# Kernel tuning notes

Hardware: AMD Instinct MI355X
Metric: run time of the kernel (lower is better)

Reference implementation:

```python
import jax, jax.numpy as jnp
import numpy as np

WS = (8, 8)          # window size
NUM_HEADS = 16
C = 512
B_ = 2048            # batch * num_windows
NW = 256             # num_windows per image (mask dim)
N = WS[0] * WS[1]    # tokens per window = 64


def _relative_position_index():
    coords = np.stack(np.meshgrid(np.arange(WS[0]), np.arange(WS[1]), indexing='ij'))  # [2,Wh,Ww]
    flat = coords.reshape(2, -1)                         # [2,N]
    rel = flat[:, :, None] - flat[:, None, :]            # [2,N,N]
    rel = rel.transpose(1, 2, 0).astype(np.int32)        # [N,N,2]
    rel[..., 0] += WS[0] - 1
    rel[..., 1] += WS[1] - 1
    rel[..., 0] *= 2 * WS[1] - 1
    return jnp.asarray(rel.sum(-1))                      # [N,N] in [0, 225)


def setup_inputs() -> dict:
    key = jax.random.key(0)
    ks = jax.random.split(key, 8)
    return {
        'x': jax.random.normal(ks[0], (B_, N, C), jnp.float32),
        'mask': jax.random.normal(ks[1], (NW, N, N), jnp.float32),
        'qkv_w': jax.random.normal(ks[2], (3 * C, C), jnp.float32) * 0.02,
        'q_bias': jax.random.normal(ks[3], (C,), jnp.float32) * 0.02,
        'v_bias': jax.random.normal(ks[4], (C,), jnp.float32) * 0.02,
        'rpb_table': jax.random.normal(ks[5], ((2 * WS[0] - 1) * (2 * WS[1] - 1), NUM_HEADS), jnp.float32) * 0.02,
        'proj_w': jax.random.normal(ks[6], (C, C), jnp.float32) * 0.02,
        'proj_b': jax.random.normal(ks[7], (C,), jnp.float32) * 0.02,
        'rel_index': _relative_position_index(),
    }


def reference(x, mask, qkv_w, q_bias, v_bias, rpb_table, proj_w, proj_b, rel_index):
    Bw, n, c = x.shape
    h = NUM_HEADS
    d = c // h
    # qkv with bias = [q_bias, 0, v_bias]
    qkv_b = jnp.concatenate([q_bias, jnp.zeros_like(v_bias), v_bias])
    qkv = x @ qkv_w.T + qkv_b                               # [B_,N,3C]
    qkv = qkv.reshape(Bw, n, 3, h, d).transpose(2, 0, 3, 1, 4)
    q, k, v = qkv[0], qkv[1], qkv[2]                        # each [B_,h,N,d]
    scale = d ** -0.5
    attn = jnp.einsum('bhnd,bhmd->bhnm', q * scale, k)      # [B_,h,N,N]
    # gathered relative position bias
    rpb = rpb_table[rel_index.reshape(-1)].reshape(n, n, h).transpose(2, 0, 1)  # [h,N,N]
    attn = attn + rpb[None]
    nW = mask.shape[0]
    attn = attn.reshape(Bw // nW, nW, h, n, n) + mask[None, :, None]
    attn = jax.nn.softmax(attn.reshape(Bw, h, n, n), axis=-1)
    out = jnp.einsum('bhnm,bhmd->bhnd', attn, v)            # [B_,h,N,d]
    out = out.transpose(0, 2, 1, 3).reshape(Bw, n, c)
    return out @ proj_w.T + proj_b
```

## Files before the change

### kernel.cpp

```cpp
#include <hip/hip_runtime.h>

typedef short s16x8 __attribute__((ext_vector_type(8)));
typedef float f32x4 __attribute__((ext_vector_type(4)));

__device__ __forceinline__ unsigned short f2bf(float f) {
    unsigned int u = __builtin_bit_cast(unsigned int, f);
    u += 0x7fffu + ((u >> 16) & 1u);
    return (unsigned short)(u >> 16);
}

__device__ __forceinline__ void gload16(const void* g, void* l) {
    __builtin_amdgcn_global_load_lds(
        (const __attribute__((address_space(1))) unsigned int*)g,
        (__attribute__((address_space(3))) unsigned int*)l,
        16, 0, 0);
}

__global__ void cast_bf16_kernel(const float* __restrict__ src,
                                 unsigned short* __restrict__ dst, int n4) {
    int i = blockIdx.x * 256 + threadIdx.x;
    if (i >= n4) return;
    float4 v = ((const float4*)src)[i];
    ushort4 o;
    o.x = f2bf(v.x); o.y = f2bf(v.y); o.z = f2bf(v.z); o.w = f2bf(v.w);
    ((ushort4*)dst)[i] = o;
}

__global__ void rpb_kernel(const float* __restrict__ table,
                           const int* __restrict__ rel,
                           float* __restrict__ rpb) {
    int t = blockIdx.x * 64 + threadIdx.x;
    int idx = rel[t];
#pragma unroll
    for (int h = 0; h < 16; ++h)
        rpb[h * 4096 + t] = table[idx * 16 + h];
}

__device__ __forceinline__ void stage_step(const unsigned short* __restrict__ Ab,
                                           const unsigned short* __restrict__ Bb,
                                           unsigned short* base, int wave,
                                           size_t gA0, size_t gA1, int k0) {
    gload16(Ab + gA0 + k0, &base[wave * 512]);
    gload16(Ab + gA1 + k0, &base[2048 + wave * 512]);
    gload16(Bb + gA0 + k0, &base[4096 + wave * 512]);
    gload16(Bb + gA1 + k0, &base[6144 + wave * 512]);
}

template <bool SW>
__device__ __forceinline__ void mfma_step(const unsigned short* base, int ln, int hk,
                                          int wr, int wc, f32x4 (&acc)[4][4]) {
    const unsigned short* Al = base;
    const unsigned short* Bl = base + 4096;
    const int sl = hk ^ ((ln >> 1) & 3);
    s16x8 af[4], bf[4];
#pragma unroll
    for (int i = 0; i < 4; ++i)
        af[i] = *(const s16x8*)&Al[(wr + i * 16 + ln) * 32 + sl * 8];
#pragma unroll
    for (int j = 0; j < 4; ++j)
        bf[j] = *(const s16x8*)&Bl[(wc + j * 16 + ln) * 32 + sl * 8];
#pragma unroll
    for (int i = 0; i < 4; ++i)
#pragma unroll
        for (int j = 0; j < 4; ++j) {
            if constexpr (SW)
                acc[j][i] = __builtin_amdgcn_mfma_f32_16x16x32_bf16(bf[j], af[i], acc[j][i], 0, 0, 0);
            else
                acc[i][j] = __builtin_amdgcn_mfma_f32_16x16x32_bf16(af[i], bf[j], acc[i][j], 0, 0, 0);
        }
}

template <bool SW>
__device__ __forceinline__ void kloop128(const unsigned short* __restrict__ Ab,
                                         const unsigned short* __restrict__ Bb,
                                         unsigned short* smem,
                                         int t, int wave, int ln, int hk,
                                         int wr, int wc, f32x4 (&acc)[4][4]) {
    const int row = t >> 2, cg = t & 3;
    const int cgs = cg ^ ((t >> 3) & 3);
    const size_t gA0 = (size_t)row * 512 + cgs * 8;
    const size_t gA1 = (size_t)(row + 64) * 512 + cgs * 8;
    unsigned short* b0 = smem;
    unsigned short* b1 = smem + 8192;

    stage_step(Ab, Bb, b0, wave, gA0, gA1, 0);
    __syncthreads();
    for (int k0 = 0; k0 < 512; k0 += 64) {
        stage_step(Ab, Bb, b1, wave, gA0, gA1, k0 + 32);
        mfma_step<SW>(b0, ln, hk, wr, wc, acc);
        __syncthreads();
        if (k0 + 64 < 512)
            stage_step(Ab, Bb, b0, wave, gA0, gA1, k0 + 64);
        mfma_step<SW>(b1, ln, hk, wr, wc, acc);
        __syncthreads();
    }
}

template <int MODE, int NCOLS>
__global__ __launch_bounds__(256) void gemm_bt(
    const unsigned short* __restrict__ A, const unsigned short* __restrict__ B,
    const float* __restrict__ bq, const float* __restrict__ bv,
    unsigned short* __restrict__ qb, unsigned short* __restrict__ kb,
    unsigned short* __restrict__ vtb,
    const float* __restrict__ pb, float* __restrict__ out) {
    __shared__ __align__(16) unsigned short smem[16384];

    constexpr int NBN = NCOLS / 128;
    const unsigned int cpx = gridDim.x >> 3;
    const unsigned int wg = (blockIdx.x & 7u) * cpx + (blockIdx.x >> 3);
    const int bm = wg / NBN;
    const int bn = wg % NBN;
    const int t = threadIdx.x;
    const int wave = t >> 6, lane = t & 63;
    const int ln = lane & 15, hk = lane >> 4;
    const int wr = (wave >> 1) * 64, wc = (wave & 1) * 64;

    const f32x4 zero = {0.f, 0.f, 0.f, 0.f};
    f32x4 acc[4][4];
#pragma unroll
    for (int i = 0; i < 4; ++i)
#pragma unroll
        for (int j = 0; j < 4; ++j) acc[i][j] = zero;

    const unsigned short* Ab = A + (size_t)bm * 128 * 512;
    const unsigned short* Bb = B + (size_t)bn * 128 * 512;

    if constexpr (MODE == 1) {
        kloop128<true>(Ab, Bb, smem, t, wave, ln, hk, wr, wc, acc);
        float* epf = (float*)smem + wave * 1280;
#pragma unroll
        for (int j = 0; j < 4; ++j) {
            const int nn0 = bn * 128 + wc + j * 16 + hk * 4;
            const float4 b4 = *(const float4*)&pb[nn0];
#pragma unroll
            for (int i = 0; i < 4; ++i) {
                const int tk = i * 16 + ln;
                float4 o4;
                o4.x = acc[j][i][0] + b4.x;
                o4.y = acc[j][i][1] + b4.y;
                o4.z = acc[j][i][2] + b4.z;
                o4.w = acc[j][i][3] + b4.w;
                *(float4*)&epf[tk * 20 + hk * 4] = o4;
            }
            const int nnb = bn * 128 + wc + j * 16;
#pragma unroll
            for (int rr = 0; rr < 4; ++rr) {
                const int li = rr * 64 + lane;
                const int tk = li >> 2, c4 = (li & 3) * 4;
                float4 v4 = *(const float4*)&epf[tk * 20 + c4];
                *(float4*)(out + (size_t)(bm * 128 + wr + tk) * NCOLS + nnb + c4) = v4;
            }
        }
    } else {
        const int which = bn >> 2;
        const int bb = bm * 2;
        const size_t winbase = (size_t)((bb + (wr >> 6)) * 16);
        unsigned short* ep = smem + wave * 2560;
        if (which < 2) {
            kloop128<true>(Ab, Bb, smem, t, wave, ln, hk, wr, wc, acc);
            unsigned short* dst0 = (which == 0) ? qb : kb;
#pragma unroll
            for (int H = 0; H < 2; ++H) {
#pragma unroll
                for (int j2 = 0; j2 < 2; ++j2) {
                    const int j = H * 2 + j2;
                    const int rem0 = (bn * 128 + wc + j * 16 + hk * 4) & 511;
                    float4 b4 = {0.f, 0.f, 0.f, 0.f};
                    if (which == 0) b4 = *(const float4*)&bq[rem0];
                    const int ch0 = j2 * 16 + hk * 4;
#pragma unroll
                    for (int i = 0; i < 4; ++i) {
                        const int tk = i * 16 + ln;
                        ushort4 pk;
                        pk.x = f2bf(acc[j][i][0] + b4.x);
                        pk.y = f2bf(acc[j][i][1] + b4.y);
                        pk.z = f2bf(acc[j][i][2] + b4.z);
                        pk.w = f2bf(acc[j][i][3] + b4.w);
                        *(ushort4*)&ep[tk * 40 + ch0] = pk;
                    }
                }
                const int remH = (bn * 128 + wc + H * 32) & 511;
                const size_t Dq = (winbase + (remH >> 5)) * 2048;
#pragma unroll
                for (int rr = 0; rr < 4; ++rr) {
                    const int li = rr * 64 + lane;
                    const int tk = li >> 2, c8 = (li & 3) * 8;
                    s16x8 val = *(const s16x8*)&ep[tk * 40 + c8];
                    *(s16x8*)(dst0 + Dq + tk * 32 + c8) = val;
                }
            }
        } else {
            kloop128<false>(Ab, Bb, smem, t, wave, ln, hk, wr, wc, acc);
#pragma unroll
            for (int H = 0; H < 2; ++H) {
#pragma unroll
                for (int j2 = 0; j2 < 2; ++j2) {
                    const int j = H * 2 + j2;
                    const int rem = (bn * 128 + wc + j * 16 + ln) & 511;
                    const float bias = bv[rem];
                    const int ch = j2 * 16 + ln;
#pragma unroll
                    for (int i = 0; i < 4; ++i) {
                        const int tk = i * 16 + hk * 4;
                        ushort4 pk;
                        pk.x = f2bf(acc[i][j][0] + bias);
                        pk.y = f2bf(acc[i][j][1] + bias);
                        pk.z = f2bf(acc[i][j][2] + bias);
                        pk.w = f2bf(acc[i][j][3] + bias);
                        *(ushort4*)&ep[ch * 72 + tk] = pk;
                    }
                }
                const int remH = (bn * 128 + wc + H * 32) & 511;
                const size_t Dv = (winbase + (remH >> 5)) * 2048;
#pragma unroll
                for (int rr = 0; rr < 4; ++rr) {
                    const int li = rr * 64 + lane;
                    const int dd = li >> 3, t8 = (li & 7) * 8;
                    s16x8 val = *(const s16x8*)&ep[dd * 72 + t8];
                    *(s16x8*)(vtb + Dv + dd * 64 + t8) = val;
                }
            }
        }
    }
}

__global__ __launch_bounds__(256) void attn_kernel(
    const unsigned short* __restrict__ qbuf, const unsigned short* __restrict__ kbuf,
    const unsigned short* __restrict__ vtbuf, const float* __restrict__ rpb,
    const float* __restrict__ mask, unsigned short* __restrict__ aout) {
    __shared__ __align__(16) unsigned short ql[64 * 32];
    __shared__ __align__(16) unsigned short kl[64 * 32];
    __shared__ __align__(16) unsigned short vl[32 * 64];
    __shared__ __align__(16) unsigned short plds[64 * 72];

    const int bh = blockIdx.x;
    const int b = bh >> 4, head = bh & 15;
    const int wmask = b & 255;
    const int t = threadIdx.x, wave = t >> 6, lane = t & 63;
    const int ln = lane & 15, hk = lane >> 4;

    const size_t base = (size_t)bh * 2048;
    {
        const int r4 = t >> 2, c4 = t & 3;
        const int qs = c4 ^ ((t >> 3) & 3);
        gload16(qbuf + base + r4 * 32 + qs * 8, &ql[wave * 512]);
        gload16(kbuf + base + r4 * 32 + qs * 8, &kl[wave * 512]);
        const int r8 = t >> 3, c8v = t & 7;
        const int vs = c8v ^ (r8 & 7);
        gload16(vtbuf + base + r8 * 64 + vs * 8, &vl[wave * 512]);
    }
    __syncthreads();

    const f32x4 zero = {0.f, 0.f, 0.f, 0.f};
    const int slq = hk ^ ((ln >> 1) & 3);
    s16x8 aq = *(const s16x8*)&ql[(wave * 16 + ln) * 32 + slq * 8];
    f32x4 sc[4];
#pragma unroll
    for (int j = 0; j < 4; ++j) {
        s16x8 bk = *(const s16x8*)&kl[(j * 16 + ln) * 32 + slq * 8];
        sc[j] = __builtin_amdgcn_mfma_f32_16x16x32_bf16(aq, bk, zero, 0, 0, 0);
    }

    const float scale = 0.17677669529663687f;
    const float* rpb_h = rpb + head * 4096;
    const float* msk = mask + wmask * 4096;

    float p[4][4];
#pragma unroll
    for (int r = 0; r < 4; ++r) {
        const int i = wave * 16 + hk * 4 + r;
        float v[4], m = -1e30f;
#pragma unroll
        for (int j = 0; j < 4; ++j) {
            const int c = j * 16 + ln;
            v[j] = sc[j][r] * scale + rpb_h[i * 64 + c] + msk[i * 64 + c];
            m = fmaxf(m, v[j]);
        }
        for (int off = 1; off < 16; off <<= 1) m = fmaxf(m, __shfl_xor(m, off));
        float s = 0.f;
#pragma unroll
        for (int j = 0; j < 4; ++j) { v[j] = __expf(v[j] - m); s += v[j]; }
        for (int off = 1; off < 16; off <<= 1) s += __shfl_xor(s, off);
        const float inv = 1.f / s;
#pragma unroll
        for (int j = 0; j < 4; ++j) p[r][j] = v[j] * inv;
    }
#pragma unroll
    for (int r = 0; r < 4; ++r)
#pragma unroll
        for (int j = 0; j < 4; ++j)
            plds[(wave * 16 + hk * 4 + r) * 72 + j * 16 + ln] = f2bf(p[r][j]);

    f32x4 o2[2] = {zero, zero};
#pragma unroll
    for (int kt = 0; kt < 2; ++kt) {
        s16x8 ap = *(const s16x8*)&plds[(wave * 16 + ln) * 72 + kt * 32 + hk * 8];
#pragma unroll
        for (int nt = 0; nt < 2; ++nt) {
            const int vsl = (kt * 4 + hk) ^ (ln & 7);
            s16x8 bvf = *(const s16x8*)&vl[(nt * 16 + ln) * 64 + vsl * 8];
            o2[nt] = __builtin_amdgcn_mfma_f32_16x16x32_bf16(bvf, ap, o2[nt], 0, 0, 0);
        }
    }
    unsigned short* ep = plds + wave * 1152;
#pragma unroll
    for (int nt = 0; nt < 2; ++nt) {
        ushort4 pk;
        pk.x = f2bf(o2[nt][0]); pk.y = f2bf(o2[nt][1]);
        pk.z = f2bf(o2[nt][2]); pk.w = f2bf(o2[nt][3]);
        *(ushort4*)&ep[ln * 40 + nt * 16 + hk * 4] = pk;
    }
    const int tk = lane >> 2, c8 = (lane & 3) * 8;
    s16x8 val = *(const s16x8*)&ep[tk * 40 + c8];
    *(s16x8*)(aout + ((size_t)(b * 64 + wave * 16 + tk)) * 512 + head * 32 + c8) = val;
}

extern "C" void kernel_launch(void* const* d_in, const int* in_sizes, int n_in,
                              void* d_out, int out_size, void* d_ws, size_t ws_size,
                              hipStream_t stream) {
    const float* x      = (const float*)d_in[0];
    const float* mask   = (const float*)d_in[1];
    const float* qkv_w  = (const float*)d_in[2];
    const float* q_bias = (const float*)d_in[3];
    const float* v_bias = (const float*)d_in[4];
    const float* rpb_t  = (const float*)d_in[5];
    const float* proj_w = (const float*)d_in[6];
    const float* proj_b = (const float*)d_in[7];
    const int*   rel    = (const int*)d_in[8];
    float* out = (float*)d_out;

    char* ws = (char*)d_ws;
    unsigned short* xbf   = (unsigned short*)ws;
    unsigned short* qbuf  = (unsigned short*)(ws + 0x08000000);
    unsigned short* kbuf  = (unsigned short*)(ws + 0x10000000);
    unsigned short* vtbuf = (unsigned short*)(ws + 0x18000000);
    unsigned short* wqkv  = (unsigned short*)(ws + 0x20000000);
    unsigned short* wproj = (unsigned short*)(ws + 0x20180000);
    float*          rpb   = (float*)(ws + 0x20200000);
    unsigned short* aout  = xbf;

    cast_bf16_kernel<<<65536, 256, 0, stream>>>(x, xbf, 16777216);
    cast_bf16_kernel<<<768, 256, 0, stream>>>(qkv_w, wqkv, 196608);
    cast_bf16_kernel<<<256, 256, 0, stream>>>(proj_w, wproj, 65536);
    rpb_kernel<<<64, 64, 0, stream>>>(rpb_t, rel, rpb);

    gemm_bt<0, 1536><<<1024 * 12, 256, 0, stream>>>(
        xbf, wqkv, q_bias, v_bias, qbuf, kbuf, vtbuf, nullptr, nullptr);

    attn_kernel<<<32768, 256, 0, stream>>>(qbuf, kbuf, vtbuf, rpb, mask, aout);

    gemm_bt<1, 512><<<1024 * 4, 256, 0, stream>>>(
        aout, wproj, nullptr, nullptr, nullptr, nullptr, nullptr, proj_b, out);
}
```

Measured before the change: 1.010 ms.

## Widen GEMM tiles to 128x256, fold q scale into epilogue, transpose softmax layout

```diff
diff --git a/kernel.cpp b/kernel.cpp
--- a/kernel.cpp
+++ b/kernel.cpp
@@ -39,73 +39,78 @@
 __device__ __forceinline__ void stage_step(const unsigned short* __restrict__ Ab,
                                            const unsigned short* __restrict__ Bb,
                                            unsigned short* base, int wave,
-                                           size_t gA0, size_t gA1, int k0) {
-    gload16(Ab + gA0 + k0, &base[wave * 512]);
-    gload16(Ab + gA1 + k0, &base[2048 + wave * 512]);
-    gload16(Bb + gA0 + k0, &base[4096 + wave * 512]);
-    gload16(Bb + gA1 + k0, &base[6144 + wave * 512]);
+                                           size_t g0, size_t g1, size_t g2,
+                                           size_t g3, int k0) {
+    gload16(Ab + g0 + k0, &base[wave * 512]);
+    gload16(Ab + g1 + k0, &base[2048 + wave * 512]);
+    gload16(Bb + g0 + k0, &base[4096 + wave * 512]);
+    gload16(Bb + g1 + k0, &base[6144 + wave * 512]);
+    gload16(Bb + g2 + k0, &base[8192 + wave * 512]);
+    gload16(Bb + g3 + k0, &base[10240 + wave * 512]);
 }
 
 template <bool SW>
 __device__ __forceinline__ void mfma_step(const unsigned short* base, int ln, int hk,
-                                          int wr, int wc, f32x4 (&acc)[4][4]) {
+                                          int wr, int wc, f32x4 (&acc)[32]) {
     const unsigned short* Al = base;
     const unsigned short* Bl = base + 4096;
     const int sl = hk ^ ((ln >> 1) & 3);
-    s16x8 af[4], bf[4];
+    s16x8 af[4], bf[8];
 #pragma unroll
     for (int i = 0; i < 4; ++i)
         af[i] = *(const s16x8*)&Al[(wr + i * 16 + ln) * 32 + sl * 8];
 #pragma unroll
-    for (int j = 0; j < 4; ++j)
+    for (int j = 0; j < 8; ++j)
         bf[j] = *(const s16x8*)&Bl[(wc + j * 16 + ln) * 32 + sl * 8];
 #pragma unroll
     for (int i = 0; i < 4; ++i)
 #pragma unroll
-        for (int j = 0; j < 4; ++j) {
+        for (int j = 0; j < 8; ++j) {
             if constexpr (SW)
-                acc[j][i] = __builtin_amdgcn_mfma_f32_16x16x32_bf16(bf[j], af[i], acc[j][i], 0, 0, 0);
+                acc[j * 4 + i] = __builtin_amdgcn_mfma_f32_16x16x32_bf16(bf[j], af[i], acc[j * 4 + i], 0, 0, 0);
             else
-                acc[i][j] = __builtin_amdgcn_mfma_f32_16x16x32_bf16(af[i], bf[j], acc[i][j], 0, 0, 0);
+                acc[i * 8 + j] = __builtin_amdgcn_mfma_f32_16x16x32_bf16(af[i], bf[j], acc[i * 8 + j], 0, 0, 0);
         }
 }
 
 template <bool SW>
-__device__ __forceinline__ void kloop128(const unsigned short* __restrict__ Ab,
-                                         const unsigned short* __restrict__ Bb,
-                                         unsigned short* smem,
-                                         int t, int wave, int ln, int hk,
-                                         int wr, int wc, f32x4 (&acc)[4][4]) {
-    const int row = t >> 2, cg = t & 3;
-    const int cgs = cg ^ ((t >> 3) & 3);
-    const size_t gA0 = (size_t)row * 512 + cgs * 8;
-    const size_t gA1 = (size_t)(row + 64) * 512 + cgs * 8;
+__device__ __forceinline__ void kloop(const unsigned short* __restrict__ Ab,
+                                      const unsigned short* __restrict__ Bb,
+                                      unsigned short* smem,
+                                      int t, int wave, int ln, int hk,
+                                      int wr, int wc, f32x4 (&acc)[32]) {
+    const int row = t >> 2;
+    const int cgs = (t & 3) ^ ((t >> 3) & 3);
+    const size_t g0 = (size_t)row * 512 + cgs * 8;
+    const size_t g1 = (size_t)(row + 64) * 512 + cgs * 8;
+    const size_t g2 = (size_t)(row + 128) * 512 + cgs * 8;
+    const size_t g3 = (size_t)(row + 192) * 512 + cgs * 8;
     unsigned short* b0 = smem;
-    unsigned short* b1 = smem + 8192;
-
-    stage_step(Ab, Bb, b0, wave, gA0, gA1, 0);
+    unsigned short* b1 = smem + 12288;
+
+    stage_step(Ab, Bb, b0, wave, g0, g1, g2, g3, 0);
     __syncthreads();
     for (int k0 = 0; k0 < 512; k0 += 64) {
-        stage_step(Ab, Bb, b1, wave, gA0, gA1, k0 + 32);
+        stage_step(Ab, Bb, b1, wave, g0, g1, g2, g3, k0 + 32);
         mfma_step<SW>(b0, ln, hk, wr, wc, acc);
         __syncthreads();
         if (k0 + 64 < 512)
-            stage_step(Ab, Bb, b0, wave, gA0, gA1, k0 + 64);
+            stage_step(Ab, Bb, b0, wave, g0, g1, g2, g3, k0 + 64);
         mfma_step<SW>(b1, ln, hk, wr, wc, acc);
         __syncthreads();
     }
 }
 
 template <int MODE, int NCOLS>
-__global__ __launch_bounds__(256) void gemm_bt(
+__global__ __launch_bounds__(256, 3) void gemm_bt(
     const unsigned short* __restrict__ A, const unsigned short* __restrict__ B,
     const float* __restrict__ bq, const float* __restrict__ bv,
     unsigned short* __restrict__ qb, unsigned short* __restrict__ kb,
     unsigned short* __restrict__ vtb,
     const float* __restrict__ pb, float* __restrict__ out) {
-    __shared__ __align__(16) unsigned short smem[16384];
-
-    constexpr int NBN = NCOLS / 128;
+    __shared__ __align__(16) unsigned short smem[24576];
+
+    constexpr int NBN = NCOLS / 256;
     const unsigned int cpx = gridDim.x >> 3;
     const unsigned int wg = (blockIdx.x & 7u) * cpx + (blockIdx.x >> 3);
     const int bm = wg / NBN;
@@ -113,36 +118,34 @@
     const int t = threadIdx.x;
     const int wave = t >> 6, lane = t & 63;
     const int ln = lane & 15, hk = lane >> 4;
-    const int wr = (wave >> 1) * 64, wc = (wave & 1) * 64;
+    const int wr = (wave >> 1) * 64, wc = (wave & 1) * 128;
 
     const f32x4 zero = {0.f, 0.f, 0.f, 0.f};
-    f32x4 acc[4][4];
-#pragma unroll
-    for (int i = 0; i < 4; ++i)
-#pragma unroll
-        for (int j = 0; j < 4; ++j) acc[i][j] = zero;
+    f32x4 acc[32];
+#pragma unroll
+    for (int i = 0; i < 32; ++i) acc[i] = zero;
 
     const unsigned short* Ab = A + (size_t)bm * 128 * 512;
-    const unsigned short* Bb = B + (size_t)bn * 128 * 512;
+    const unsigned short* Bb = B + (size_t)bn * 256 * 512;
 
     if constexpr (MODE == 1) {
-        kloop128<true>(Ab, Bb, smem, t, wave, ln, hk, wr, wc, acc);
+        kloop<true>(Ab, Bb, smem, t, wave, ln, hk, wr, wc, acc);
         float* epf = (float*)smem + wave * 1280;
 #pragma unroll
-        for (int j = 0; j < 4; ++j) {
-            const int nn0 = bn * 128 + wc + j * 16 + hk * 4;
+        for (int j = 0; j < 8; ++j) {
+            const int nn0 = bn * 256 + wc + j * 16 + hk * 4;
             const float4 b4 = *(const float4*)&pb[nn0];
 #pragma unroll
             for (int i = 0; i < 4; ++i) {
                 const int tk = i * 16 + ln;
                 float4 o4;
-                o4.x = acc[j][i][0] + b4.x;
-                o4.y = acc[j][i][1] + b4.y;
-                o4.z = acc[j][i][2] + b4.z;
-                o4.w = acc[j][i][3] + b4.w;
+                o4.x = acc[j * 4 + i][0] + b4.x;
+                o4.y = acc[j * 4 + i][1] + b4.y;
+                o4.z = acc[j * 4 + i][2] + b4.z;
+                o4.w = acc[j * 4 + i][3] + b4.w;
                 *(float4*)&epf[tk * 20 + hk * 4] = o4;
             }
-            const int nnb = bn * 128 + wc + j * 16;
+            const int nnb = bn * 256 + wc + j * 16;
 #pragma unroll
             for (int rr = 0; rr < 4; ++rr) {
                 const int li = rr * 64 + lane;
@@ -152,19 +155,20 @@
             }
         }
     } else {
-        const int which = bn >> 2;
+        const int which = bn >> 1;
         const int bb = bm * 2;
         const size_t winbase = (size_t)((bb + (wr >> 6)) * 16);
         unsigned short* ep = smem + wave * 2560;
         if (which < 2) {
-            kloop128<true>(Ab, Bb, smem, t, wave, ln, hk, wr, wc, acc);
+            kloop<true>(Ab, Bb, smem, t, wave, ln, hk, wr, wc, acc);
             unsigned short* dst0 = (which == 0) ? qb : kb;
-#pragma unroll
-            for (int H = 0; H < 2; ++H) {
+            const float qsc = (which == 0) ? 0.17677669529663687f : 1.f;
+#pragma unroll
+            for (int Q = 0; Q < 4; ++Q) {
 #pragma unroll
                 for (int j2 = 0; j2 < 2; ++j2) {
-                    const int j = H * 2 + j2;
-                    const int rem0 = (bn * 128 + wc + j * 16 + hk * 4) & 511;
+                    const int j = Q * 2 + j2;
+                    const int rem0 = (bn & 1) * 256 + wc + j * 16 + hk * 4;
                     float4 b4 = {0.f, 0.f, 0.f, 0.f};
                     if (which == 0) b4 = *(const float4*)&bq[rem0];
                     const int ch0 = j2 * 16 + hk * 4;
@@ -172,15 +176,15 @@
                     for (int i = 0; i < 4; ++i) {
                         const int tk = i * 16 + ln;
                         ushort4 pk;
-                        pk.x = f2bf(acc[j][i][0] + b4.x);
-                        pk.y = f2bf(acc[j][i][1] + b4.y);
-                        pk.z = f2bf(acc[j][i][2] + b4.z);
-                        pk.w = f2bf(acc[j][i][3] + b4.w);
+                        pk.x = f2bf((acc[j * 4 + i][0] + b4.x) * qsc);
+                        pk.y = f2bf((acc[j * 4 + i][1] + b4.y) * qsc);
+                        pk.z = f2bf((acc[j * 4 + i][2] + b4.z) * qsc);
+                        pk.w = f2bf((acc[j * 4 + i][3] + b4.w) * qsc);
                         *(ushort4*)&ep[tk * 40 + ch0] = pk;
                     }
                 }
-                const int remH = (bn * 128 + wc + H * 32) & 511;
-                const size_t Dq = (winbase + (remH >> 5)) * 2048;
+                const int remQ = (bn & 1) * 256 + wc + Q * 32;
+                const size_t Dq = (winbase + (remQ >> 5)) * 2048;
 #pragma unroll
                 for (int rr = 0; rr < 4; ++rr) {
                     const int li = rr * 64 + lane;
@@ -190,28 +194,28 @@
                 }
             }
         } else {
-            kloop128<false>(Ab, Bb, smem, t, wave, ln, hk, wr, wc, acc);
-#pragma unroll
-            for (int H = 0; H < 2; ++H) {
+            kloop<false>(Ab, Bb, smem, t, wave, ln, hk, wr, wc, acc);
+#pragma unroll
+            for (int Q = 0; Q < 4; ++Q) {
 #pragma unroll
                 for (int j2 = 0; j2 < 2; ++j2) {
-                    const int j = H * 2 + j2;
-                    const int rem = (bn * 128 + wc + j * 16 + ln) & 511;
+                    const int j = Q * 2 + j2;
+                    const int rem = (bn & 1) * 256 + wc + j * 16 + ln;
                     const float bias = bv[rem];
                     const int ch = j2 * 16 + ln;
 #pragma unroll
                     for (int i = 0; i < 4; ++i) {
                         const int tk = i * 16 + hk * 4;
                         ushort4 pk;
-                        pk.x = f2bf(acc[i][j][0] + bias);
-                        pk.y = f2bf(acc[i][j][1] + bias);
-                        pk.z = f2bf(acc[i][j][2] + bias);
-                        pk.w = f2bf(acc[i][j][3] + bias);
+                        pk.x = f2bf(acc[i * 8 + j][0] + bias);
+                        pk.y = f2bf(acc[i * 8 + j][1] + bias);
+                        pk.z = f2bf(acc[i * 8 + j][2] + bias);
+                        pk.w = f2bf(acc[i * 8 + j][3] + bias);
                         *(ushort4*)&ep[ch * 72 + tk] = pk;
                     }
                 }
-                const int remH = (bn * 128 + wc + H * 32) & 511;
-                const size_t Dv = (winbase + (remH >> 5)) * 2048;
+                const int remQ = (bn & 1) * 256 + wc + Q * 32;
+                const size_t Dv = (winbase + (remQ >> 5)) * 2048;
 #pragma unroll
                 for (int rr = 0; rr < 4; ++rr) {
                     const int li = rr * 64 + lane;
@@ -258,38 +262,46 @@
 #pragma unroll
     for (int j = 0; j < 4; ++j) {
         s16x8 bk = *(const s16x8*)&kl[(j * 16 + ln) * 32 + slq * 8];
-        sc[j] = __builtin_amdgcn_mfma_f32_16x16x32_bf16(aq, bk, zero, 0, 0, 0);
-    }
-
-    const float scale = 0.17677669529663687f;
-    const float* rpb_h = rpb + head * 4096;
-    const float* msk = mask + wmask * 4096;
+        sc[j] = __builtin_amdgcn_mfma_f32_16x16x32_bf16(bk, aq, zero, 0, 0, 0);
+    }
+
+    const int q = wave * 16 + ln;
+    const float4* rp4 = (const float4*)(rpb + head * 4096);
+    const float4* mk4 = (const float4*)(mask + wmask * 4096);
 
     float p[4][4];
-#pragma unroll
-    for (int r = 0; r < 4; ++r) {
-        const int i = wave * 16 + hk * 4 + r;
-        float v[4], m = -1e30f;
-#pragma unroll
-        for (int j = 0; j < 4; ++j) {
-            const int c = j * 16 + ln;
-            v[j] = sc[j][r] * scale + rpb_h[i * 64 + c] + msk[i * 64 + c];
-            m = fmaxf(m, v[j]);
-        }
-        for (int off = 1; off < 16; off <<= 1) m = fmaxf(m, __shfl_xor(m, off));
-        float s = 0.f;
-#pragma unroll
-        for (int j = 0; j < 4; ++j) { v[j] = __expf(v[j] - m); s += v[j]; }
-        for (int off = 1; off < 16; off <<= 1) s += __shfl_xor(s, off);
-        const float inv = 1.f / s;
-#pragma unroll
-        for (int j = 0; j < 4; ++j) p[r][j] = v[j] * inv;
-    }
-#pragma unroll
-    for (int r = 0; r < 4; ++r)
-#pragma unroll
-        for (int j = 0; j < 4; ++j)
-            plds[(wave * 16 + hk * 4 + r) * 72 + j * 16 + ln] = f2bf(p[r][j]);
+    float m = -1e30f;
+#pragma unroll
+    for (int j = 0; j < 4; ++j) {
+        const float4 rb = rp4[q * 16 + j * 4 + hk];
+        const float4 mk = mk4[q * 16 + j * 4 + hk];
+        p[j][0] = sc[j][0] + rb.x + mk.x;
+        p[j][1] = sc[j][1] + rb.y + mk.y;
+        p[j][2] = sc[j][2] + rb.z + mk.z;
+        p[j][3] = sc[j][3] + rb.w + mk.w;
+#pragma unroll
+        for (int r = 0; r < 4; ++r) m = fmaxf(m, p[j][r]);
+    }
+    m = fmaxf(m, __shfl_xor(m, 16));
+    m = fmaxf(m, __shfl_xor(m, 32));
+    float s = 0.f;
+#pragma unroll
+    for (int j = 0; j < 4; ++j)
+#pragma unroll
+        for (int r = 0; r < 4; ++r) { p[j][r] = __expf(p[j][r] - m); s += p[j][r]; }
+    s += __shfl_xor(s, 16);
+    s += __shfl_xor(s, 32);
+    const float inv = 1.f / s;
+
+#pragma unroll
+    for (int j = 0; j < 4; ++j) {
+        ushort4 pk;
+        pk.x = f2bf(p[j][0] * inv);
+        pk.y = f2bf(p[j][1] * inv);
+        pk.z = f2bf(p[j][2] * inv);
+        pk.w = f2bf(p[j][3] * inv);
+        *(ushort4*)&plds[q * 72 + j * 16 + hk * 4] = pk;
+    }
 
     f32x4 o2[2] = {zero, zero};
 #pragma unroll
@@ -344,11 +356,11 @@
     cast_bf16_kernel<<<256, 256, 0, stream>>>(proj_w, wproj, 65536);
     rpb_kernel<<<64, 64, 0, stream>>>(rpb_t, rel, rpb);
 
-    gemm_bt<0, 1536><<<1024 * 12, 256, 0, stream>>>(
+    gemm_bt<0, 1536><<<6144, 256, 0, stream>>>(
         xbf, wqkv, q_bias, v_bias, qbuf, kbuf, vtbuf, nullptr, nullptr);
 
     attn_kernel<<<32768, 256, 0, stream>>>(qbuf, kbuf, vtbuf, rpb, mask, aout);
 
-    gemm_bt<1, 512><<<1024 * 4, 256, 0, stream>>>(
+    gemm_bt<1, 512><<<2048, 256, 0, stream>>>(
         aout, wproj, nullptr, nullptr, nullptr, nullptr, nullptr, proj_b, out);
 }
```

Measured after the change: 1.976 ms. 1.96x slower.
